# Kernel optimization log

Hardware: AMD Instinct MI355X
Metric: run time of the kernel (lower is better)

Reference implementation:

```python
import jax, jax.numpy as jnp
import numpy as np

R = 64                      # grid resolution
SCALE = 1.05                # half-extent of the grid
C = 64                      # feature_dim
N = 500_000                 # number of query positions
GRID_SIZE = SCALE * 2.0 / R


def _build_grid():
    """Regular (R+1)^3 vertex grid spanning [-SCALE, SCALE]^3 plus per-cube
    8-corner vertex indices, with binary corner ordering c = 4*dx + 2*dy + dz
    so corner 7-c is the diagonally opposite corner (needed for flip(-2))."""
    R1 = R + 1
    lin = (np.arange(R1, dtype=np.float32) / R - 0.5) * (2.0 * SCALE)
    gx, gy, gz = np.meshgrid(lin, lin, lin, indexing='ij')
    vertices = np.stack([gx, gy, gz], axis=-1).reshape(-1, 3)  # [(R+1)^3, 3]
    i, j, k = np.meshgrid(np.arange(R), np.arange(R), np.arange(R), indexing='ij')
    corners = []
    for c in range(8):
        dx, dy, dz = (c >> 2) & 1, (c >> 1) & 1, c & 1
        corners.append((i + dx) * R1 * R1 + (j + dy) * R1 + (k + dz))
    grid_indices = np.stack(corners, axis=-1).astype(np.int32)  # [R, R, R, 8]
    return jnp.asarray(vertices), jnp.asarray(grid_indices)


def setup_inputs() -> dict:
    key = jax.random.key(0)
    k1, k2 = jax.random.split(key)
    vertices, grid_indices = _build_grid()
    # query positions uniform in [-SCALE, SCALE]^3
    positions = (jax.random.uniform(k1, (N, 3), dtype=jnp.float32) * 2.0 - 1.0) * SCALE
    # learned feature grid, init like torch.randn(...) * init_std
    feats = jax.random.normal(k2, ((R + 1) ** 3, C), dtype=jnp.float32) * 0.001
    return {"positions": positions, "feats": feats,
            "vertices": vertices, "grid_indices": grid_indices}


def reference(positions, feats, vertices, grid_indices):
    # NeuFAM.trilinear_query
    x = jnp.clip((positions / (2.0 * SCALE) + 0.5) * R, 0.0, float(R))
    nearest = jnp.clip(jnp.floor(x).astype(jnp.int32), 0, R - 1)          # [N, 3]
    idx = grid_indices[nearest[:, 0], nearest[:, 1], nearest[:, 2]]       # [N, 8]
    verts = vertices[idx]                                                 # [N, 8, 3]
    nf = feats[idx]                                                       # [N, 8, C]
    # trilinear weight = prod over xyz of |p - opposite corner| / grid_size
    w = jnp.prod(jnp.abs((positions[:, None, :] - verts[:, ::-1, :]) / GRID_SIZE), axis=-1)  # [N, 8]
    return jnp.einsum('nkc,nk->nc', nf, w)                                # [N, C]
```

## Files before the change

kernel.cpp:

```cpp
#include <hip/hip_runtime.h>
#include <hip/hip_fp16.h>


#define GRID_R    64
#define GRID_R1   65
#define NCHAN     64
#define NVERT     (GRID_R1 * GRID_R1 * GRID_R1)
#define FEAT_ELEMS ((size_t)NVERT * NCHAN)

typedef float    f32x4 __attribute__((ext_vector_type(4)));
typedef _Float16 f16x8 __attribute__((ext_vector_type(8)));

__global__ __launch_bounds__(256) void convert_kernel(
    const f32x4* __restrict__ in,
    f16x8* __restrict__ out,
    int n8)
{
    int i = blockIdx.x * 256 + threadIdx.x;
    if (i >= n8) return;
    f32x4 a = in[2 * i];
    f32x4 b = in[2 * i + 1];
    f16x8 h;
    h[0] = (_Float16)a.x; h[1] = (_Float16)a.y;
    h[2] = (_Float16)a.z; h[3] = (_Float16)a.w;
    h[4] = (_Float16)b.x; h[5] = (_Float16)b.y;
    h[6] = (_Float16)b.z; h[7] = (_Float16)b.w;
    __builtin_nontemporal_store(h, &out[i]);
}

__global__ __launch_bounds__(256) void trilerp_f16_kernel(
    const float* __restrict__ pos,
    const f16x8* __restrict__ feats,
    f32x4* __restrict__ out4,
    int n)
{
    const int tid = blockIdx.x * 256 + threadIdx.x;
    const int pt  = tid >> 3;
    if (pt >= n) return;
    const int sub = tid & 7;

    const float px = pos[pt * 3 + 0];
    const float py = pos[pt * 3 + 1];
    const float pz = pos[pt * 3 + 2];

    float x = (px / 2.1f + 0.5f) * 64.0f;
    float y = (py / 2.1f + 0.5f) * 64.0f;
    float z = (pz / 2.1f + 0.5f) * 64.0f;
    x = fminf(fmaxf(x, 0.0f), 64.0f);
    y = fminf(fmaxf(y, 0.0f), 64.0f);
    z = fminf(fmaxf(z, 0.0f), 64.0f);
    int ci = min((int)x, GRID_R - 1);
    int cj = min((int)y, GRID_R - 1);
    int ck = min((int)z, GRID_R - 1);

    const float INV_GS = 64.0f / 2.1f;
    float vx0 = ((float)ci       * 0.015625f - 0.5f) * 2.1f;
    float vx1 = ((float)(ci + 1) * 0.015625f - 0.5f) * 2.1f;
    float vy0 = ((float)cj       * 0.015625f - 0.5f) * 2.1f;
    float vy1 = ((float)(cj + 1) * 0.015625f - 0.5f) * 2.1f;
    float vz0 = ((float)ck       * 0.015625f - 0.5f) * 2.1f;
    float vz1 = ((float)(ck + 1) * 0.015625f - 0.5f) * 2.1f;

    float wx1 = fabsf(px - vx0) * INV_GS;
    float wx0 = fabsf(px - vx1) * INV_GS;
    float wy1 = fabsf(py - vy0) * INV_GS;
    float wy0 = fabsf(py - vy1) * INV_GS;
    float wz1 = fabsf(pz - vz0) * INV_GS;
    float wz0 = fabsf(pz - vz1) * INV_GS;

    const int RS = NCHAN / 8;
    const int SY = GRID_R1 * RS;
    const int SX = GRID_R1 * GRID_R1 * RS;
    int base = ((ci * GRID_R1 + cj) * GRID_R1 + ck) * RS + sub;

    f16x8 f000 = feats[base];
    f16x8 f001 = feats[base + RS];
    f16x8 f010 = feats[base + SY];
    f16x8 f011 = feats[base + SY + RS];
    f16x8 f100 = feats[base + SX];
    f16x8 f101 = feats[base + SX + RS];
    f16x8 f110 = feats[base + SX + SY];
    f16x8 f111 = feats[base + SX + SY + RS];

    float w000 = wx0 * wy0 * wz0, w001 = wx0 * wy0 * wz1;
    float w010 = wx0 * wy1 * wz0, w011 = wx0 * wy1 * wz1;
    float w100 = wx1 * wy0 * wz0, w101 = wx1 * wy0 * wz1;
    float w110 = wx1 * wy1 * wz0, w111 = wx1 * wy1 * wz1;

    f32x4 acc0 = {0.f, 0.f, 0.f, 0.f};
    f32x4 acc1 = {0.f, 0.f, 0.f, 0.f};
#define ACCUM(F, W)                                                  \
    { acc0.x += (float)F[0] * W; acc0.y += (float)F[1] * W;          \
      acc0.z += (float)F[2] * W; acc0.w += (float)F[3] * W;          \
      acc1.x += (float)F[4] * W; acc1.y += (float)F[5] * W;          \
      acc1.z += (float)F[6] * W; acc1.w += (float)F[7] * W; }
    ACCUM(f000, w000) ACCUM(f001, w001) ACCUM(f010, w010) ACCUM(f011, w011)
    ACCUM(f100, w100) ACCUM(f101, w101) ACCUM(f110, w110) ACCUM(f111, w111)
#undef ACCUM

    __builtin_nontemporal_store(acc0, &out4[pt * 16 + sub * 2]);
    __builtin_nontemporal_store(acc1, &out4[pt * 16 + sub * 2 + 1]);
}

__global__ __launch_bounds__(256) void trilerp_f32_kernel(
    const float* __restrict__ pos,
    const f32x4* __restrict__ feats4,
    f32x4* __restrict__ out4,
    int n)
{
    const int tid = blockIdx.x * 256 + threadIdx.x;
    const int pt  = tid >> 4;
    if (pt >= n) return;
    const int sub = tid & 15;

    const float px = pos[pt * 3 + 0];
    const float py = pos[pt * 3 + 1];
    const float pz = pos[pt * 3 + 2];

    float x = (px / 2.1f + 0.5f) * 64.0f;
    float y = (py / 2.1f + 0.5f) * 64.0f;
    float z = (pz / 2.1f + 0.5f) * 64.0f;
    x = fminf(fmaxf(x, 0.0f), 64.0f);
    y = fminf(fmaxf(y, 0.0f), 64.0f);
    z = fminf(fmaxf(z, 0.0f), 64.0f);
    int ci = min((int)x, GRID_R - 1);
    int cj = min((int)y, GRID_R - 1);
    int ck = min((int)z, GRID_R - 1);

    const float INV_GS = 64.0f / 2.1f;
    float vx0 = ((float)ci       * 0.015625f - 0.5f) * 2.1f;
    float vx1 = ((float)(ci + 1) * 0.015625f - 0.5f) * 2.1f;
    float vy0 = ((float)cj       * 0.015625f - 0.5f) * 2.1f;
    float vy1 = ((float)(cj + 1) * 0.015625f - 0.5f) * 2.1f;
    float vz0 = ((float)ck       * 0.015625f - 0.5f) * 2.1f;
    float vz1 = ((float)(ck + 1) * 0.015625f - 0.5f) * 2.1f;

    float wx1 = fabsf(px - vx0) * INV_GS;
    float wx0 = fabsf(px - vx1) * INV_GS;
    float wy1 = fabsf(py - vy0) * INV_GS;
    float wy0 = fabsf(py - vy1) * INV_GS;
    float wz1 = fabsf(pz - vz0) * INV_GS;
    float wz0 = fabsf(pz - vz1) * INV_GS;

    const int RS = 16, SY = GRID_R1 * RS, SX = GRID_R1 * GRID_R1 * RS;
    int base = ((ci * GRID_R1 + cj) * GRID_R1 + ck) * RS + sub;

    f32x4 f000 = feats4[base];
    f32x4 f001 = feats4[base + RS];
    f32x4 f010 = feats4[base + SY];
    f32x4 f011 = feats4[base + SY + RS];
    f32x4 f100 = feats4[base + SX];
    f32x4 f101 = feats4[base + SX + RS];
    f32x4 f110 = feats4[base + SX + SY];
    f32x4 f111 = feats4[base + SX + SY + RS];

    float w000 = wx0 * wy0 * wz0, w001 = wx0 * wy0 * wz1;
    float w010 = wx0 * wy1 * wz0, w011 = wx0 * wy1 * wz1;
    float w100 = wx1 * wy0 * wz0, w101 = wx1 * wy0 * wz1;
    float w110 = wx1 * wy1 * wz0, w111 = wx1 * wy1 * wz1;

    f32x4 acc = f000 * w000 + f001 * w001 + f010 * w010 + f011 * w011
              + f100 * w100 + f101 * w101 + f110 * w110 + f111 * w111;

    __builtin_nontemporal_store(acc, &out4[pt * 16 + sub]);
}

extern "C" void kernel_launch(void* const* d_in, const int* in_sizes, int n_in,
                              void* d_out, int out_size, void* d_ws, size_t ws_size,
                              hipStream_t stream) {
    const float* pos   = (const float*)d_in[0];
    const float* feats = (const float*)d_in[1];
    f32x4* out4 = (f32x4*)d_out;

    const int n = in_sizes[0] / 3;
    const size_t need = FEAT_ELEMS * sizeof(_Float16);

    if (ws_size >= need) {
        f16x8* feats16 = (f16x8*)d_ws;
        const int n8 = (int)(FEAT_ELEMS / 8);
        convert_kernel<<<(n8 + 255) / 256, 256, 0, stream>>>(
            (const f32x4*)feats, feats16, n8);
        const long long total = (long long)n * 8;
        trilerp_f16_kernel<<<(int)((total + 255) / 256), 256, 0, stream>>>(
            pos, feats16, out4, n);
    } else {
        const long long total = (long long)n * 16;
        trilerp_f32_kernel<<<(int)((total + 255) / 256), 256, 0, stream>>>(
            pos, (const f32x4*)feats, out4, n);
    }
}
```

Measured before the change: 108.4 us.

## Bin query points into spatial superblocks before trilinear gather for locality

Adds a counting-sort pipeline. A histogram of 8x8x8-cell superbins is fused into the fp16 convert kernel, then an exclusive scan, an atomic scatter of (position, index) records, and a sorted trilerp kernel that writes results back to each point's original index. Spatially nearby points now gather the same feature rows together, which is meant to improve L2 hit rate. Blocks are also remapped across 8 groups, apparently to spread contiguous bins across XCDs. The cost is extra launches, a memset, atomics and a round trip of the records buffer.

```diff
diff --git a/kernel.cpp b/kernel.cpp
--- a/kernel.cpp
+++ b/kernel.cpp
@@ -2,56 +2,112 @@
 #include <hip/hip_fp16.h>
 
 
-#define GRID_R    64
-#define GRID_R1   65
-#define NCHAN     64
-#define NVERT     (GRID_R1 * GRID_R1 * GRID_R1)
+#define GRID_R     64
+#define GRID_R1    65
+#define NCHAN      64
+#define NVERT      (GRID_R1 * GRID_R1 * GRID_R1)
 #define FEAT_ELEMS ((size_t)NVERT * NCHAN)
+#define NBINS      512
 
 typedef float    f32x4 __attribute__((ext_vector_type(4)));
 typedef _Float16 f16x8 __attribute__((ext_vector_type(8)));
 
-__global__ __launch_bounds__(256) void convert_kernel(
-    const f32x4* __restrict__ in,
-    f16x8* __restrict__ out,
-    int n8)
-{
-    int i = blockIdx.x * 256 + threadIdx.x;
-    if (i >= n8) return;
-    f32x4 a = in[2 * i];
-    f32x4 b = in[2 * i + 1];
-    f16x8 h;
-    h[0] = (_Float16)a.x; h[1] = (_Float16)a.y;
-    h[2] = (_Float16)a.z; h[3] = (_Float16)a.w;
-    h[4] = (_Float16)b.x; h[5] = (_Float16)b.y;
-    h[6] = (_Float16)b.z; h[7] = (_Float16)b.w;
-    __builtin_nontemporal_store(h, &out[i]);
-}
-
-__global__ __launch_bounds__(256) void trilerp_f16_kernel(
-    const float* __restrict__ pos,
-    const f16x8* __restrict__ feats,
-    f32x4* __restrict__ out4,
-    int n)
-{
-    const int tid = blockIdx.x * 256 + threadIdx.x;
-    const int pt  = tid >> 3;
-    if (pt >= n) return;
-    const int sub = tid & 7;
-
-    const float px = pos[pt * 3 + 0];
-    const float py = pos[pt * 3 + 1];
-    const float pz = pos[pt * 3 + 2];
-
+__device__ __forceinline__ void cell_of(float px, float py, float pz,
+                                        int& ci, int& cj, int& ck) {
     float x = (px / 2.1f + 0.5f) * 64.0f;
     float y = (py / 2.1f + 0.5f) * 64.0f;
     float z = (pz / 2.1f + 0.5f) * 64.0f;
     x = fminf(fmaxf(x, 0.0f), 64.0f);
     y = fminf(fmaxf(y, 0.0f), 64.0f);
     z = fminf(fmaxf(z, 0.0f), 64.0f);
-    int ci = min((int)x, GRID_R - 1);
-    int cj = min((int)y, GRID_R - 1);
-    int ck = min((int)z, GRID_R - 1);
+    ci = min((int)x, GRID_R - 1);
+    cj = min((int)y, GRID_R - 1);
+    ck = min((int)z, GRID_R - 1);
+}
+
+__device__ __forceinline__ int sbin_of(int ci, int cj, int ck) {
+    return ((ci >> 3) << 6) | ((cj >> 3) << 3) | (ck >> 3);
+}
+
+__global__ __launch_bounds__(256) void convert_hist_kernel(
+    const f32x4* __restrict__ in,
+    f16x8* __restrict__ outF,
+    const float* __restrict__ pos,
+    int* __restrict__ hist,
+    int n8, int n)
+{
+    int i = blockIdx.x * 256 + threadIdx.x;
+    if (i < n8) {
+        f32x4 a = in[2 * i];
+        f32x4 b = in[2 * i + 1];
+        f16x8 h;
+        h[0] = (_Float16)a.x; h[1] = (_Float16)a.y;
+        h[2] = (_Float16)a.z; h[3] = (_Float16)a.w;
+        h[4] = (_Float16)b.x; h[5] = (_Float16)b.y;
+        h[6] = (_Float16)b.z; h[7] = (_Float16)b.w;
+        __builtin_nontemporal_store(h, &outF[i]);
+    }
+    if (i < n) {
+        int ci, cj, ck;
+        cell_of(pos[i * 3], pos[i * 3 + 1], pos[i * 3 + 2], ci, cj, ck);
+        atomicAdd(&hist[sbin_of(ci, cj, ck)], 1);
+    }
+}
+
+__global__ __launch_bounds__(NBINS) void scan_kernel(
+    const int* __restrict__ hist, int* __restrict__ cursor)
+{
+    __shared__ int s[NBINS];
+    const int t = threadIdx.x;
+    int own = hist[t];
+    s[t] = own;
+    __syncthreads();
+    for (int off = 1; off < NBINS; off <<= 1) {
+        int v = (t >= off) ? s[t - off] : 0;
+        __syncthreads();
+        s[t] += v;
+        __syncthreads();
+    }
+    cursor[t] = s[t] - own;
+}
+
+__global__ __launch_bounds__(256) void scatter_kernel(
+    const float* __restrict__ pos,
+    int* __restrict__ cursor,
+    f32x4* __restrict__ records,
+    int n)
+{
+    int i = blockIdx.x * 256 + threadIdx.x;
+    if (i >= n) return;
+    float px = pos[i * 3], py = pos[i * 3 + 1], pz = pos[i * 3 + 2];
+    int ci, cj, ck;
+    cell_of(px, py, pz, ci, cj, ck);
+    int slot = atomicAdd(&cursor[sbin_of(ci, cj, ck)], 1);
+    f32x4 r = {px, py, pz, __int_as_float(i)};
+    records[slot] = r;
+}
+
+__global__ __launch_bounds__(256) void trilerp_sorted_kernel(
+    const f32x4* __restrict__ records,
+    const f16x8* __restrict__ feats,
+    f32x4* __restrict__ out4,
+    int n, int nwg)
+{
+    const int o  = blockIdx.x;
+    const int x  = o & 7, oo = o >> 3;
+    const int q  = nwg >> 3, r = nwg & 7;
+    const int vb = (x < r ? x * (q + 1) : r * (q + 1) + (x - r) * q) + oo;
+
+    const int slot = vb * 32 + (threadIdx.x >> 3);
+    if (slot >= n) return;
+    const int sub = threadIdx.x & 7;
+
+    const f32x4 rec = records[slot];
+    const float px = rec.x, py = rec.y, pz = rec.z;
+    const int orig = __float_as_int(rec.w);
+
+    int ci, cj, ck;
+    cell_of(px, py, pz, ci, cj, ck);
 
     const float INV_GS = 64.0f / 2.1f;
     float vx0 = ((float)ci       * 0.015625f - 0.5f) * 2.1f;
@@ -98,6 +154,68 @@
     ACCUM(f100, w100) ACCUM(f101, w101) ACCUM(f110, w110) ACCUM(f111, w111)
 #undef ACCUM
 
+    __builtin_nontemporal_store(acc0, &out4[orig * 16 + sub * 2]);
+    __builtin_nontemporal_store(acc1, &out4[orig * 16 + sub * 2 + 1]);
+}
+
+__global__ __launch_bounds__(256) void trilerp_f16_kernel(
+    const float* __restrict__ pos,
+    const f16x8* __restrict__ feats,
+    f32x4* __restrict__ out4,
+    int n)
+{
+    const int tid = blockIdx.x * 256 + threadIdx.x;
+    const int pt  = tid >> 3;
+    if (pt >= n) return;
+    const int sub = tid & 7;
+
+    const float px = pos[pt * 3], py = pos[pt * 3 + 1], pz = pos[pt * 3 + 2];
+    int ci, cj, ck;
+    cell_of(px, py, pz, ci, cj, ck);
+
+    const float INV_GS = 64.0f / 2.1f;
+    float vx0 = ((float)ci       * 0.015625f - 0.5f) * 2.1f;
+    float vx1 = ((float)(ci + 1) * 0.015625f - 0.5f) * 2.1f;
+    float vy0 = ((float)cj       * 0.015625f - 0.5f) * 2.1f;
+    float vy1 = ((float)(cj + 1) * 0.015625f - 0.5f) * 2.1f;
+    float vz0 = ((float)ck       * 0.015625f - 0.5f) * 2.1f;
+    float vz1 = ((float)(ck + 1) * 0.015625f - 0.5f) * 2.1f;
+
+    float wx1 = fabsf(px - vx0) * INV_GS;
+    float wx0 = fabsf(px - vx1) * INV_GS;
+    float wy1 = fabsf(py - vy0) * INV_GS;
+    float wy0 = fabsf(py - vy1) * INV_GS;
+    float wz1 = fabsf(pz - vz0) * INV_GS;
+    float wz0 = fabsf(pz - vz1) * INV_GS;
+
+    const int RS = NCHAN / 8, SY = GRID_R1 * RS, SX = GRID_R1 * GRID_R1 * RS;
+    int base = ((ci * GRID_R1 + cj) * GRID_R1 + ck) * RS + sub;
+
+    f16x8 f000 = feats[base];
+    f16x8 f001 = feats[base + RS];
+    f16x8 f010 = feats[base + SY];
+    f16x8 f011 = feats[base + SY + RS];
+    f16x8 f100 = feats[base + SX];
+    f16x8 f101 = feats[base + SX + RS];
+    f16x8 f110 = feats[base + SX + SY];
+    f16x8 f111 = feats[base + SX + SY + RS];
+
+    float w000 = wx0 * wy0 * wz0, w001 = wx0 * wy0 * wz1;
+    float w010 = wx0 * wy1 * wz0, w011 = wx0 * wy1 * wz1;
+    float w100 = wx1 * wy0 * wz0, w101 = wx1 * wy0 * wz1;
+    float w110 = wx1 * wy1 * wz0, w111 = wx1 * wy1 * wz1;
+
+    f32x4 acc0 = {0.f, 0.f, 0.f, 0.f};
+    f32x4 acc1 = {0.f, 0.f, 0.f, 0.f};
+#define ACCUM(F, W)                                                  \
+    { acc0.x += (float)F[0] * W; acc0.y += (float)F[1] * W;          \
+      acc0.z += (float)F[2] * W; acc0.w += (float)F[3] * W;          \
+      acc1.x += (float)F[4] * W; acc1.y += (float)F[5] * W;          \
+      acc1.z += (float)F[6] * W; acc1.w += (float)F[7] * W; }
+    ACCUM(f000, w000) ACCUM(f001, w001) ACCUM(f010, w010) ACCUM(f011, w011)
+    ACCUM(f100, w100) ACCUM(f101, w101) ACCUM(f110, w110) ACCUM(f111, w111)
+#undef ACCUM
+
     __builtin_nontemporal_store(acc0, &out4[pt * 16 + sub * 2]);
     __builtin_nontemporal_store(acc1, &out4[pt * 16 + sub * 2 + 1]);
 }
@@ -113,19 +231,9 @@
     if (pt >= n) return;
     const int sub = tid & 15;
 
-    const float px = pos[pt * 3 + 0];
-    const float py = pos[pt * 3 + 1];
-    const float pz = pos[pt * 3 + 2];
-
-    float x = (px / 2.1f + 0.5f) * 64.0f;
-    float y = (py / 2.1f + 0.5f) * 64.0f;
-    float z = (pz / 2.1f + 0.5f) * 64.0f;
-    x = fminf(fmaxf(x, 0.0f), 64.0f);
-    y = fminf(fmaxf(y, 0.0f), 64.0f);
-    z = fminf(fmaxf(z, 0.0f), 64.0f);
-    int ci = min((int)x, GRID_R - 1);
-    int cj = min((int)y, GRID_R - 1);
-    int ck = min((int)z, GRID_R - 1);
+    const float px = pos[pt * 3], py = pos[pt * 3 + 1], pz = pos[pt * 3 + 2];
+    int ci, cj, ck;
+    cell_of(px, py, pz, ci, cj, ck);
 
     const float INV_GS = 64.0f / 2.1f;
     float vx0 = ((float)ci       * 0.015625f - 0.5f) * 2.1f;
@@ -172,14 +280,41 @@
     const float* feats = (const float*)d_in[1];
     f32x4* out4 = (f32x4*)d_out;
 
-    const int n = in_sizes[0] / 3;
-    const size_t need = FEAT_ELEMS * sizeof(_Float16);
-
-    if (ws_size >= need) {
+    const int n  = in_sizes[0] / 3;
+    const int n8 = (int)(FEAT_ELEMS / 8);
+
+    const size_t featBytes = FEAT_ELEMS * sizeof(_Float16);
+    const size_t offF = 0;
+    const size_t offR = (featBytes + 127) & ~(size_t)127;
+    const size_t offH = offR + (size_t)n * 16;
+    const size_t offC = offH + NBINS * sizeof(int);
+    const size_t needSorted = offC + NBINS * sizeof(int);
+
+    if (ws_size >= needSorted) {
+        char* ws = (char*)d_ws;
+        f16x8* feats16 = (f16x8*)(ws + offF);
+        f32x4* records = (f32x4*)(ws + offR);
+        int*   hist    = (int*)(ws + offH);
+        int*   cursor  = (int*)(ws + offC);
+
+        hipMemsetAsync(hist, 0, NBINS * sizeof(int), stream);
+
+        const int k1_blocks = (n8 + 255) / 256;
+        convert_hist_kernel<<<k1_blocks, 256, 0, stream>>>(
+            (const f32x4*)feats, feats16, pos, hist, n8, n);
+
+        scan_kernel<<<1, NBINS, 0, stream>>>(hist, cursor);
+
+        scatter_kernel<<<(n + 255) / 256, 256, 0, stream>>>(
+            pos, cursor, records, n);
+
+        const int nwg = (n + 31) / 32;
+        trilerp_sorted_kernel<<<nwg, 256, 0, stream>>>(
+            records, feats16, out4, n, nwg);
+    } else if (ws_size >= featBytes) {
         f16x8* feats16 = (f16x8*)d_ws;
-        const int n8 = (int)(FEAT_ELEMS / 8);
-        convert_kernel<<<(n8 + 255) / 256, 256, 0, stream>>>(
-            (const f32x4*)feats, feats16, n8);
+        convert_hist_kernel<<<(n8 + 255) / 256, 256, 0, stream>>>(
+            (const f32x4*)feats, feats16, nullptr, nullptr, n8, 0);
         const long long total = (long long)n * 8;
         trilerp_f16_kernel<<<(int)((total + 255) / 256), 256, 0, stream>>>(
             pos, feats16, out4, n);
```

Result: slower. 387.0 us (+256.9%).
